# Optimization experiments

Measured on AMD Instinct MI355X. Metric: run time of the kernel, lower is better.

The kernel has to match this reference:

```python
import jax, jax.numpy as jnp
import numpy as np

B, N, E, ATT, TT, IT = 32, 5000, 500, 50, 4, 24
TEMP = 0.5

def leaky(x):
    return jnp.where(x > 0, x, 0.1 * x)

def ln(x, g, b, eps=1e-5):
    m = jnp.mean(x, axis=-1, keepdims=True)
    v = jnp.mean((x - m) ** 2, axis=-1, keepdims=True)
    return (x - m) * jax.lax.rsqrt(v + eps) * g + b

def setup_inputs() -> dict:
    key = jax.random.key(0)
    ks = jax.random.split(key, 16)
    s = 0.05
    return {
        'positive_sample': jax.random.randint(ks[0], (B, 3), 0, N),
        'ent_text_emb': jax.random.normal(ks[1], (N, TT, 384), jnp.float32),
        'ent_img_emb': jax.random.normal(ks[2], (N, IT, 383), jnp.float32),
        'entity_embedding': jax.random.normal(ks[3], (N, E), jnp.float32) * s,
        'relation_embedding': jax.random.normal(ks[4], (N, E), jnp.float32) * s,
        'W_text': jax.random.normal(ks[5], (ATT, 384), jnp.float32) * s,
        'b_text': jnp.zeros((ATT,), jnp.float32),
        'W_img': jax.random.normal(ks[6], (ATT, 383), jnp.float32) * s,
        'b_img': jnp.zeros((ATT,), jnp.float32),
        'W_tproj': jax.random.normal(ks[7], (ATT, ATT * IT), jnp.float32) * s,
        'b_tproj': jnp.zeros((ATT,), jnp.float32),
        'W_iproj': jax.random.normal(ks[8], (ATT, ATT * TT), jnp.float32) * s,
        'b_iproj': jnp.zeros((ATT,), jnp.float32),
        'W_rel1': jax.random.normal(ks[9], (IT * TT, E), jnp.float32) * s,
        'b_rel1': jnp.zeros((IT * TT,), jnp.float32),
        'W_rel2': jax.random.normal(ks[10], (IT * TT, E), jnp.float32) * s,
        'b_rel2': jnp.zeros((IT * TT,), jnp.float32),
        'W1': jax.random.normal(ks[11], (100, 2 * E), jnp.float32) * s,
        'b1': jnp.zeros((100,), jnp.float32),
        'W3': jax.random.normal(ks[12], (E, 100), jnp.float32) * s,
        'b3': jnp.zeros((E,), jnp.float32),
        'ln_g': jnp.ones((ATT,), jnp.float32),
        'ln_b': jnp.zeros((ATT,), jnp.float32),
    }

def _cos_sim(X, p):
    # X [B,N,d], p [B,d]; denominators are detached as in the torch code
    num = jnp.einsum('bnd,bd->bn', X, p)
    den = jnp.linalg.norm(X, axis=2) * jnp.linalg.norm(p, axis=1)[:, None]
    return num / (jax.lax.stop_gradient(den) + 1e-10)

def reference(positive_sample, ent_text_emb, ent_img_emb, entity_embedding,
              relation_embedding, W_text, b_text, W_img, b_img, W_tproj, b_tproj,
              W_iproj, b_iproj, W_rel1, b_rel1, W_rel2, b_rel2, W1, b1, W3, b3,
              ln_g, ln_b):
    rel = relation_embedding[positive_sample[:, 1]]              # [B,E]
    text_emb = leaky(jnp.einsum('ntf,df->ntd', ent_text_emb, W_text) + b_text)  # [N,4,50]
    img_emb = leaky(jnp.einsum('nif,df->nid', ent_img_emb, W_img) + b_img)      # [N,24,50]
    cross = jnp.einsum('nid,ntd->nit', img_emb, text_emb)        # [N,24,4]

    # image branch: softmax over img tokens, plus relation-gated path
    img_att = jnp.einsum('nti,nid->ntd', jax.nn.softmax(cross.transpose(0, 2, 1), axis=2), img_emb)  # [N,4,50]
    rg_i = jax.nn.sigmoid(rel @ W_rel1.T + b_rel1).reshape(B, IT, TT)           # [B,24,4]
    gated_i = rg_i[:, None] * cross[None]                                        # [B,N,24,4]
    img_att_rg = jnp.einsum('bnit,nid->bntd', gated_i, img_emb)                  # [B,N,4,50]
    img_att_all = ln(img_att_rg, ln_g, ln_b) + ln(img_att, ln_g, ln_b)[None]
    img_att_all = img_att_all.reshape(B, N, TT * ATT) @ W_iproj.T + b_iproj      # [B,N,50]

    # text branch: softmax over text tokens, plus relation-gated path
    text_att = jnp.einsum('nit,ntd->nid', jax.nn.softmax(cross, axis=2), text_emb)  # [N,24,50]
    rg_t = jax.nn.sigmoid(rel @ W_rel2.T + b_rel2).reshape(B, IT, TT)
    gated_t = rg_t[:, None] * cross[None]                                        # [B,N,24,4]
    text_att_rg = jnp.einsum('bnit,ntd->bnid', gated_t, text_emb)                # [B,N,24,50]
    text_att_all = ln(text_att_rg, ln_g, ln_b) + ln(text_att, ln_g, ln_b)[None]
    text_att_all = text_att_all.reshape(B, N, IT * ATT) @ W_tproj.T + b_tproj    # [B,N,50]

    # structural gate on KGE entity embeddings (split W1 to avoid concat)
    h = leaky(entity_embedding @ W1[:, :E].T[None].squeeze(0).T.T  # placeholder removed below
              ) if False else None
    h = leaky((entity_embedding @ W1[:, :E].T)[None] + (rel @ W1[:, E:].T)[:, None] + b1)  # [B,N,100]
    gate = jax.nn.sigmoid(h @ W3.T + b3)                                         # [B,N,E]
    t_att = entity_embedding[None] * gate                                        # [B,N,E]

    pos_idx = positive_sample[:, 2]  # tail-batch
    bi = jnp.arange(B)
    pos_img = img_att_all[bi, pos_idx]    # [B,50]
    pos_text = text_att_all[bi, pos_idx]  # [B,50]
    pos_t = t_att[bi, pos_idx]            # [B,E]

    simil_img = _cos_sim(img_att_all, pos_img)
    simil_text = _cos_sim(text_att_all, pos_text)
    simil_t = _cos_sim(t_att, pos_t)

    out = (jax.nn.softmax(simil_t / TEMP, axis=1)
           + jax.nn.softmax(simil_img / TEMP, axis=1)
           + jax.nn.softmax(simil_text / TEMP, axis=1))
    return (out, simil_img, simil_text, simil_t)
```

## Files before the change

### kernel.cpp

```cpp
#include <hip/hip_runtime.h>
#include <math.h>

#define BB 32
#define NN 5000
#define EE 500
#define AT 50
#define TTT 4
#define ITT 24
#define FT 384
#define FI 383
#define KH 100
#define BN (BB*NN)

__device__ __forceinline__ float leaky(float x){ return x > 0.f ? x : 0.1f*x; }
__device__ __forceinline__ float sigm(float x){ return 1.f/(1.f+__expf(-x)); }

enum : size_t {
  O_WTT = 0,
  O_WIT = 19968,
  O_WIP = 39936,
  O_WTP = 50336,
  O_W1T = 112736,
  O_W3T = 162736,
  O_SIP = 212736,
  O_STP = 212944,
  O_CBI = 214192,
  O_CBT = 214244,
  O_RGI = 214296,
  O_RGT = 217368,
  O_RB  = 220440,
  O_A   = 223640,
  O_PT  = 723640,
  O_PTN = 739640,
  O_PIM = 739672,
  O_PIMN= 741336,
  O_PTX = 741368,
  O_PTXN= 743032,
  O_MR  = 743064,
  O_SR  = 743160,
  O_EMB = 743256,
};

__global__ void k_prep(const float* Wt, const float* Wi, const float* Wip, const float* Wtp,
                       const float* W1, const float* W3, const float* g, const float* lb,
                       const float* bip, const float* btp, float* ws){
  int id = blockIdx.x*256 + threadIdx.x;
  if (id < 19968){ int f=id/52, d=id%52; ws[O_WTT+id] = (d<50)? Wt[d*FT+f] : 0.f; return; }
  id -= 19968;
  if (id < 19968){ int f=id/52, d=id%52; ws[O_WIT+id] = (f<383 && d<50)? Wi[d*FI+f] : 0.f; return; }
  id -= 19968;
  if (id < 10400){ int m=id/52, o=id%52; int t=m/50, d=m%50;
                   ws[O_WIP+id] = (o<50)? Wip[o*200+t*50+d]*g[d] : 0.f; return; }
  id -= 10400;
  if (id < 62400){ int m=id/52, o=id%52; int i=m/50, d=m%50;
                   ws[O_WTP+id] = (o<50)? Wtp[o*1200+i*50+d]*g[d] : 0.f; return; }
  id -= 62400;
  if (id < 50000){ int e=id/100, k=id%100; ws[O_W1T+id] = W1[k*1000+e]; return; }
  id -= 50000;
  if (id < 50000){ int k=id/500, e=id%500; ws[O_W3T+id] = W3[e*100+k]; return; }
  id -= 50000;
  if (id < 208){ int t=id/52, o=id%52; float s=0;
                 if (o<50) for(int d=0;d<50;d++) s += Wip[o*200+t*50+d]*g[d];
                 ws[O_SIP+id]=s; return; }
  id -= 208;
  if (id < 1248){ int i=id/52, o=id%52; float s=0;
                  if (o<50) for(int d=0;d<50;d++) s += Wtp[o*1200+i*50+d]*g[d];
                  ws[O_STP+id]=s; return; }
  id -= 1248;
  if (id < 52){ int o=id; float s=0;
                if (o<50){ for(int j=0;j<200;j++) s += lb[j%50]*Wip[o*200+j]; s=2.f*s+bip[o]; }
                ws[O_CBI+o]=s; return; }
  id -= 52;
  if (id < 52){ int o=id; float s=0;
                if (o<50){ for(int j=0;j<1200;j++) s += lb[j%50]*Wtp[o*1200+j]; s=2.f*s+btp[o]; }
                ws[O_CBT+o]=s; return; }
}

__global__ void k_rel(const int* ps, const float* rele, const float* Wr1, const float* br1,
                      const float* Wr2, const float* br2, const float* W1, float* ws){
  __shared__ float relL[EE];
  int b = blockIdx.x;
  int r = ps[b*3+1];
  for (int e=threadIdx.x; e<EE; e+=256) relL[e] = rele[(size_t)r*EE+e];
  __syncthreads();
  for (int j=threadIdx.x; j<292; j+=256){
    if (j<96){
      float a=br1[j]; const float* w=&Wr1[j*EE];
      for(int e=0;e<EE;e++) a+=relL[e]*w[e];
      ws[O_RGI+b*96+j]=sigm(a);
    } else if (j<192){
      int jj=j-96; float a=br2[jj]; const float* w=&Wr2[jj*EE];
      for(int e=0;e<EE;e++) a+=relL[e]*w[e];
      ws[O_RGT+b*96+jj]=sigm(a);
    } else {
      int k=j-192; float a=0; const float* w=&W1[k*1000+500];
      for(int e=0;e<EE;e++) a+=relL[e]*w[e];
      ws[O_RB+b*100+k]=a;
    }
  }
}

__global__ void k_A(const float* ent, float* ws){
  __shared__ float entL[8*EE];
  int n0 = blockIdx.x*8;
  for (int idx=threadIdx.x; idx<8*EE; idx+=256) entL[idx] = ent[(size_t)n0*EE + idx];
  __syncthreads();
  const float* W1T = &ws[O_W1T];
  for (int idx=threadIdx.x; idx<800; idx+=256){
    int rr=idx/100, k=idx%100; float a=0;
    const float* el=&entL[rr*EE];
    for (int e=0;e<EE;e++) a += el[e]*W1T[e*100+k];
    ws[O_A + (size_t)(n0+rr)*100 + k] = a;
  }
}

__global__ void k_pos(const int* ps, const float* ent, const float* b1, const float* b3, float* ws){
  __shared__ float hL[KH];
  __shared__ float red[4];
  int b=blockIdx.x; int n=ps[b*3+2]; int tid=threadIdx.x;
  if (tid<KH) hL[tid] = leaky(ws[O_A+(size_t)n*100+tid] + ws[O_RB+b*100+tid] + b1[tid]);
  __syncthreads();
  const float* w3t=&ws[O_W3T];
  float sq=0;
  for (int e=tid; e<EE; e+=256){
    float a=b3[e];
    for (int k=0;k<KH;k++) a += hL[k]*w3t[k*500+e];
    float gg=sigm(a); float ta=ent[(size_t)n*EE+e]*gg;
    ws[O_PT+b*500+e]=ta; sq+=ta*ta;
  }
  for (int off=1; off<64; off<<=1) sq += __shfl_xor(sq, off);
  if ((tid&63)==0) red[tid>>6]=sq;
  __syncthreads();
  if (tid==0) ws[O_PTN+b] = sqrtf(red[0]+red[1]+red[2]+red[3]);
}

__global__ __launch_bounds__(256) void k_emb(const float* X, const float* Wp, const float* bias,
                                             float* emb, int R, int F, int rowsPerN, int rowOff,
                                             int xstride){
  __shared__ __align__(16) float Wl[128*52];
  int row = blockIdx.x*256 + threadIdx.x;
  bool act = row < R;
  float4 acc[13];
  #pragma unroll
  for (int c=0;c<13;c++) acc[c]=make_float4(0,0,0,0);
  const float* xr = X + (size_t)(act?row:0)*xstride;
  for (int f0=0; f0<F; f0+=128){
    int nf = min(128, F-f0);
    __syncthreads();
    for (int j=threadIdx.x; j<nf*52; j+=256) Wl[j] = Wp[(size_t)f0*52 + j];
    __syncthreads();
    if (act){
      for (int f=0; f<nf; ++f){
        float x = xr[f0+f];
        const float4* wr = (const float4*)&Wl[f*52];
        #pragma unroll
        for (int c=0;c<13;++c){
          float4 w=wr[c];
          acc[c].x+=x*w.x; acc[c].y+=x*w.y; acc[c].z+=x*w.z; acc[c].w+=x*w.w;
        }
      }
    }
  }
  if (act){
    int n = row / rowsPerN, rr = row % rowsPerN;
    float* dst = emb + (size_t)n*1456 + (size_t)(rowOff+rr)*52;
    #pragma unroll
    for (int c=0;c<13;++c){
      float4 v=acc[c]; int o=c*4;
      v.x=leaky(v.x+bias[o]); v.y=leaky(v.y+bias[o+1]);
      if (c<12){ v.z=leaky(v.z+bias[o+2]); v.w=leaky(v.w+bias[o+3]); }
      else { v.z=0.f; v.w=0.f; }
      *(float4*)&dst[o]=v;
    }
  }
}

__global__ __launch_bounds__(256) void k_main(const int* ps, float* ws, float* out, int mode){
  __shared__ __align__(16) float teie[1456];
  __shared__ __align__(16) float Pm[120*52];
  __shared__ __align__(16) float Um[120*32];
  __shared__ __align__(16) float Gi[576];
  __shared__ __align__(16) float crs[96];
  __shared__ __align__(16) float aimg[96], atxt[96];
  __shared__ __align__(16) float part1[96], part2[96];
  __shared__ __align__(16) float aU[120];
  __shared__ __align__(16) float PattC[52], QattC[52];
  __shared__ float Gts[16], mimg[24], mtxt[4];
  __shared__ float muA1[4], muA2[24];
  __shared__ float accD1[32], accN1[32], accD2[32], accN2[32];

  int tid = threadIdx.x;
  int bstar = blockIdx.x;
  int n = mode ? ps[bstar*3+2] : blockIdx.x;

  const float* embn = &ws[O_EMB + (size_t)n*1456];
  for (int j=tid; j<364; j+=256) *(float4*)&teie[j*4] = *(const float4*)&embn[j*4];
  if (tid<32){ accD1[tid]=0.f; accN1[tid]=0.f; accD2[tid]=0.f; accN2[tid]=0.f; }
  __syncthreads();

  for (int it=tid; it<716; it+=256){
    if (it<576){
      int i=it/24, j=it%24; float s=0;
      const float* a=&teie[(4+i)*52]; const float* b=&teie[(4+j)*52];
      for(int d=0;d<50;d++) s+=a[d]*b[d];
      Gi[it]=s;
    } else if (it<672){
      int c=it-576; int i=c>>2, t=c&3; float s=0;
      const float* a=&teie[(4+i)*52]; const float* b=&teie[t*52];
      for(int d=0;d<50;d++) s+=a[d]*b[d];
      crs[c]=s;
    } else if (it<688){
      int c=it-672; int t=c>>2, u=c&3; float s=0;
      const float* a=&teie[t*52]; const float* b=&teie[u*52];
      for(int d=0;d<50;d++) s+=a[d]*b[d];
      Gts[c]=s;
    } else if (it<712){
      int i=it-688; float s=0; const float* a=&teie[(4+i)*52];
      for(int d=0;d<50;d++) s+=a[d];
      mimg[i]=s*0.02f;
    } else {
      int t=it-712; float s=0; const float* a=&teie[t*52];
      for(int d=0;d<50;d++) s+=a[d];
      mtxt[t]=s*0.02f;
    }
  }
  __syncthreads();

  if (tid<4){
    int t=tid;
    float mx=-1e30f; for(int i=0;i<24;i++) mx=fmaxf(mx,crs[i*4+t]);
    float ex[24]; float s=0;
    for(int i=0;i<24;i++){ ex[i]=__expf(crs[i*4+t]-mx); s+=ex[i]; }
    float inv=1.f/s; float mu=0;
    for(int i=0;i<24;i++){ float a=ex[i]*inv; aimg[i*4+t]=a; mu+=a*mimg[i]; }
    muA1[t]=mu;
  } else if (tid>=64 && tid<88){
    int i=tid-64;
    float mx=-1e30f; for(int t=0;t<4;t++) mx=fmaxf(mx,crs[i*4+t]);
    float ex[4]; float s=0;
    for(int t=0;t<4;t++){ ex[t]=__expf(crs[i*4+t]-mx); s+=ex[t]; }
    float inv=1.f/s; float mu=0;
    for(int t=0;t<4;t++){ float a=ex[t]*inv; atxt[i*4+t]=a; mu+=a*mtxt[t]; }
    muA2[i]=mu;
  }
  __syncthreads();

  const float* WIPg=&ws[O_WIP];
  for (int it=tid; it<1248; it+=256){
    int z=it/13, q=it%13; int t=z/24, i=z%24;
    const float* wb=&WIPg[(size_t)(t*50)*52 + q*4];
    const float* ieb=&teie[(4+i)*52];
    float4 a=make_float4(0,0,0,0);
    for (int d=0; d<50; ++d){
      float e=ieb[d];
      float4 w=*(const float4*)&wb[(size_t)d*52];
      a.x+=e*w.x; a.y+=e*w.y; a.z+=e*w.z; a.w+=e*w.w;
    }
    *(float4*)&Pm[z*52+q*4]=a;
  }
  for (int j=tid; j<208; j+=256) Pm[96*52+j]=ws[O_SIP+j];
  if (tid<96){
    int i=tid>>2, t=tid&3;
    float s=0; for(int j=0;j<24;j++) s+=Gi[i*24+j]*aimg[j*4+t];
    part1[tid]=aimg[tid]*s;
  } else if (tid<192){
    int c=tid-96; int t=c&3;
    float s=0; for(int u=0;u<4;u++) s+=Gts[t*4+u]*atxt[(c&~3)+u];
    part2[c]=atxt[c]*s;
  }
  __syncthreads();

  if (tid<128){
    int b=tid&31, t=tid>>5;
    float w1r[24];
    for(int i=0;i<24;i++) w1r[i]=ws[O_RGI+b*96+i*4+t]*crs[i*4+t];
    float mu=0; for(int i=0;i<24;i++) mu+=w1r[i]*mimg[i];
    float q=0;
    for(int i=0;i<24;i++){ float s=0; for(int j=0;j<24;j++) s+=Gi[i*24+j]*w1r[j]; q+=w1r[i]*s; }
    float inv=rsqrtf(q*0.02f-mu*mu+1e-5f);
    for(int i=0;i<24;i++) Um[(t*24+i)*32+b]=inv*w1r[i];
    Um[(96+t)*32+b]=-inv*mu;
  } else if (tid<228){
    int z=tid-128;
    int t=(z<96)? (z/24) : (z-96);
    float q=0; for(int i=0;i<24;i++) q+=part1[i*4+t];
    float inv=rsqrtf(q*0.02f-muA1[t]*muA1[t]+1e-5f);
    aU[z]=(z<96)? inv*aimg[(z%24)*4+t] : -inv*muA1[t];
  }
  __syncthreads();

  if (tid<52){
    float s=ws[O_CBI+tid];
    for(int z=0;z<100;z++) s+=aU[z]*Pm[z*52+tid];
    PattC[tid]=s;
  }
  __syncthreads();

  {
    int b=tid&31, q0=tid>>5;
    bool h2=(q0+8)<13;
    float4 a0=make_float4(0,0,0,0), a1=make_float4(0,0,0,0);
    #pragma unroll 4
    for (int z=0; z<100; ++z){
      float u=Um[z*32+b];
      float4 p0=*(const float4*)&Pm[z*52+q0*4];
      a0.x+=u*p0.x; a0.y+=u*p0.y; a0.z+=u*p0.z; a0.w+=u*p0.w;
      if (h2){
        float4 p1=*(const float4*)&Pm[z*52+(q0+8)*4];
        a1.x+=u*p1.x; a1.y+=u*p1.y; a1.z+=u*p1.z; a1.w+=u*p1.w;
      }
    }
    float4 c0=*(const float4*)&PattC[q0*4];
    a0.x+=c0.x; a0.y+=c0.y; a0.z+=c0.z; a0.w+=c0.w;
    if (h2){ float4 c1=*(const float4*)&PattC[(q0+8)*4]; a1.x+=c1.x; a1.y+=c1.y; a1.z+=c1.z; a1.w+=c1.w; }
    float ni=a0.x*a0.x+a0.y*a0.y+a0.z*a0.z+a0.w*a0.w;
    if (h2) ni+=a1.x*a1.x+a1.y*a1.y+a1.z*a1.z+a1.w*a1.w;
    if (!mode){
      const float* pv=&ws[O_PIM+b*52];
      float4 p0=*(const float4*)&pv[q0*4];
      float di=a0.x*p0.x+a0.y*p0.y+a0.z*p0.z+a0.w*p0.w;
      if (h2){
        float4 p1=*(const float4*)&pv[(q0+8)*4];
        di+=a1.x*p1.x+a1.y*p1.y+a1.z*p1.z+a1.w*p1.w;
      }
      atomicAdd(&accD1[b],di); atomicAdd(&accN1[b],ni);
    } else {
      atomicAdd(&accN1[b],ni);
      if (b==bstar){
        *(float4*)&ws[O_PIM+b*52+q0*4]=a0;
        if (h2) *(float4*)&ws[O_PIM+b*52+(q0+8)*4]=a1;
      }
    }
  }
  __syncthreads();

  if (!mode){
    if (tid<32)
      out[(size_t)BN + (size_t)tid*NN + n] = accD1[tid]/(sqrtf(accN1[tid])*ws[O_PIMN+tid]+1e-10f);
  } else {
    if (tid==0) ws[O_PIMN+bstar]=sqrtf(accN1[bstar]);
  }
  {
    const float* WTPg=&ws[O_WTP];
    for (int it=tid; it<1248; it+=256){
      int z=it/13, q=it%13; int t=z/24, i=z%24;
      const float* wb=&WTPg[(size_t)(i*50)*52 + q*4];
      const float* teb=&teie[t*52];
      float4 a=make_float4(0,0,0,0);
      for (int d=0; d<50; ++d){
        float e=teb[d];
        float4 w=*(const float4*)&wb[(size_t)d*52];
        a.x+=e*w.x; a.y+=e*w.y; a.z+=e*w.z; a.w+=e*w.w;
      }
      *(float4*)&Pm[z*52+q*4]=a;
    }
    for (int j=tid; j<1248; j+=256) Pm[96*52+j]=ws[O_STP+j];
  }
  __syncthreads();

  for (int it=tid; it<888; it+=256){
    if (it<768){
      int b=it&31, i=it>>5;
      float w2r[4];
      for(int t=0;t<4;t++) w2r[t]=ws[O_RGT+b*96+i*4+t]*crs[i*4+t];
      float mu=0; for(int t=0;t<4;t++) mu+=w2r[t]*mtxt[t];
      float q=0;
      for(int t=0;t<4;t++){ float s=0; for(int u=0;u<4;u++) s+=Gts[t*4+u]*w2r[u]; q+=w2r[t]*s; }
      float inv=rsqrtf(q*0.02f-mu*mu+1e-5f);
      for(int t=0;t<4;t++) Um[(t*24+i)*32+b]=inv*w2r[t];
      Um[(96+i)*32+b]=-inv*mu;
    } else {
      int z=it-768;
      int i=(z<96)? (z%24) : (z-96);
      float q=0; for(int t=0;t<4;t++) q+=part2[i*4+t];
      float inv=rsqrtf(q*0.02f-muA2[i]*muA2[i]+1e-5f);
      aU[z]=(z<96)? inv*atxt[(z%24)*4+(z/24)] : -inv*muA2[i];
    }
  }
  __syncthreads();

  if (tid<52){
    float s=ws[O_CBT+tid];
    for(int z=0;z<120;z++) s+=aU[z]*Pm[z*52+tid];
    QattC[tid]=s;
  }
  __syncthreads();

  {
    int b=tid&31, q0=tid>>5;
    bool h2=(q0+8)<13;
    float4 a0=make_float4(0,0,0,0), a1=make_float4(0,0,0,0);
    #pragma unroll 4
    for (int z=0; z<120; ++z){
      float u=Um[z*32+b];
      float4 p0=*(const float4*)&Pm[z*52+q0*4];
      a0.x+=u*p0.x; a0.y+=u*p0.y; a0.z+=u*p0.z; a0.w+=u*p0.w;
      if (h2){
        float4 p1=*(const float4*)&Pm[z*52+(q0+8)*4];
        a1.x+=u*p1.x; a1.y+=u*p1.y; a1.z+=u*p1.z; a1.w+=u*p1.w;
      }
    }
    float4 c0=*(const float4*)&QattC[q0*4];
    a0.x+=c0.x; a0.y+=c0.y; a0.z+=c0.z; a0.w+=c0.w;
    if (h2){ float4 c1=*(const float4*)&QattC[(q0+8)*4]; a1.x+=c1.x; a1.y+=c1.y; a1.z+=c1.z; a1.w+=c1.w; }
    float ni=a0.x*a0.x+a0.y*a0.y+a0.z*a0.z+a0.w*a0.w;
    if (h2) ni+=a1.x*a1.x+a1.y*a1.y+a1.z*a1.z+a1.w*a1.w;
    if (!mode){
      const float* pv=&ws[O_PTX+b*52];
      float4 p0=*(const float4*)&pv[q0*4];
      float di=a0.x*p0.x+a0.y*p0.y+a0.z*p0.z+a0.w*p0.w;
      if (h2){
        float4 p1=*(const float4*)&pv[(q0+8)*4];
        di+=a1.x*p1.x+a1.y*p1.y+a1.z*p1.z+a1.w*p1.w;
      }
      atomicAdd(&accD2[b],di); atomicAdd(&accN2[b],ni);
    } else {
      atomicAdd(&accN2[b],ni);
      if (b==bstar){
        *(float4*)&ws[O_PTX+b*52+q0*4]=a0;
        if (h2) *(float4*)&ws[O_PTX+b*52+(q0+8)*4]=a1;
      }
    }
  }
  __syncthreads();

  if (!mode){
    if (tid<32)
      out[2*(size_t)BN + (size_t)tid*NN + n] = accD2[tid]/(sqrtf(accN2[tid])*ws[O_PTXN+tid]+1e-10f);
  } else {
    if (tid==0) ws[O_PTXN+bstar]=sqrtf(accN2[bstar]);
  }
}

__global__ __launch_bounds__(256) void k_gate(const float* ent, const float* b1, const float* b3,
                                              float* ws, float* out){
  __shared__ float entL[EE];
  __shared__ float b3L[EE];
  __shared__ __align__(16) float hallT[KH*32];
  __shared__ __align__(16) float w3c[KH*100];
  __shared__ __align__(16) float PTc[BB*100];
  __shared__ float numL[BB], sqL[BB];
  int n=blockIdx.x, tid=threadIdx.x;

  for (int e=tid; e<EE; e+=256){ entL[e]=ent[(size_t)n*EE+e]; b3L[e]=b3[e]; }
  if (tid<BB){ numL[tid]=0.f; sqL[tid]=0.f; }
  for (int idx=tid; idx<KH*32; idx+=256){
    int k=idx>>5, b=idx&31;
    hallT[idx] = leaky(ws[O_A+(size_t)n*KH+k] + ws[O_RB+b*KH+k] + b1[k]);
  }

  int eslot=tid&31, bslot=tid>>5;
  bool val = eslot<25;
  int j0 = (val? eslot:0)*4;
  float pn0=0,pn1=0,pn2=0,pn3=0, ps0=0,ps1=0,ps2=0,ps3=0;
  const float* W3T=&ws[O_W3T];
  const float* PT=&ws[O_PT];

  for (int c=0;c<5;c++){
    __syncthreads();
    for (int idx=tid; idx<10000; idx+=256){
      int k=idx/100, j=idx%100;
      w3c[idx]=W3T[(size_t)k*500 + c*100 + j];
    }
    for (int idx=tid; idx<3200; idx+=256){
      int b=idx/100, j=idx%100;
      PTc[idx]=PT[(size_t)b*EE + c*100 + j];
    }
    __syncthreads();

    float4 a0=make_float4(0,0,0,0), a1=make_float4(0,0,0,0);
    float4 a2=make_float4(0,0,0,0), a3=make_float4(0,0,0,0);
    const float4* wr=(const float4*)&w3c[j0];
    const float4* hr=(const float4*)&hallT[bslot*4];
    #pragma unroll 4
    for (int k=0;k<KH;k++){
      float4 w=wr[(size_t)k*25];
      float4 h=hr[(size_t)k*8];
      a0.x+=h.x*w.x; a0.y+=h.x*w.y; a0.z+=h.x*w.z; a0.w+=h.x*w.w;
      a1.x+=h.y*w.x; a1.y+=h.y*w.y; a1.z+=h.y*w.z; a1.w+=h.y*w.w;
      a2.x+=h.z*w.x; a2.y+=h.z*w.y; a2.z+=h.z*w.z; a2.w+=h.z*w.w;
      a3.x+=h.w*w.x; a3.y+=h.w*w.y; a3.z+=h.w*w.z; a3.w+=h.w*w.w;
    }
    if (val){
      float4 bb4=*(const float4*)&b3L[c*100+j0];
      float4 ee4=*(const float4*)&entL[c*100+j0];
      float4 p0=*(const float4*)&PTc[(bslot*4+0)*100+j0];
      float4 p1=*(const float4*)&PTc[(bslot*4+1)*100+j0];
      float4 p2=*(const float4*)&PTc[(bslot*4+2)*100+j0];
      float4 p3=*(const float4*)&PTc[(bslot*4+3)*100+j0];
      float t;
      t=ee4.x*sigm(a0.x+bb4.x); pn0+=t*p0.x; ps0+=t*t;
      t=ee4.y*sigm(a0.y+bb4.y); pn0+=t*p0.y; ps0+=t*t;
      t=ee4.z*sigm(a0.z+bb4.z); pn0+=t*p0.z; ps0+=t*t;
      t=ee4.w*sigm(a0.w+bb4.w); pn0+=t*p0.w; ps0+=t*t;
      t=ee4.x*sigm(a1.x+bb4.x); pn1+=t*p1.x; ps1+=t*t;
      t=ee4.y*sigm(a1.y+bb4.y); pn1+=t*p1.y; ps1+=t*t;
      t=ee4.z*sigm(a1.z+bb4.z); pn1+=t*p1.z; ps1+=t*t;
      t=ee4.w*sigm(a1.w+bb4.w); pn1+=t*p1.w; ps1+=t*t;
      t=ee4.x*sigm(a2.x+bb4.x); pn2+=t*p2.x; ps2+=t*t;
      t=ee4.y*sigm(a2.y+bb4.y); pn2+=t*p2.y; ps2+=t*t;
      t=ee4.z*sigm(a2.z+bb4.z); pn2+=t*p2.z; ps2+=t*t;
      t=ee4.w*sigm(a2.w+bb4.w); pn2+=t*p2.w; ps2+=t*t;
      t=ee4.x*sigm(a3.x+bb4.x); pn3+=t*p3.x; ps3+=t*t;
      t=ee4.y*sigm(a3.y+bb4.y); pn3+=t*p3.y; ps3+=t*t;
      t=ee4.z*sigm(a3.z+bb4.z); pn3+=t*p3.z; ps3+=t*t;
      t=ee4.w*sigm(a3.w+bb4.w); pn3+=t*p3.w; ps3+=t*t;
    }
  }
  for (int off=1; off<32; off<<=1){
    pn0+=__shfl_xor(pn0,off); ps0+=__shfl_xor(ps0,off);
    pn1+=__shfl_xor(pn1,off); ps1+=__shfl_xor(ps1,off);
    pn2+=__shfl_xor(pn2,off); ps2+=__shfl_xor(ps2,off);
    pn3+=__shfl_xor(pn3,off); ps3+=__shfl_xor(ps3,off);
  }
  if (eslot==0){
    int b0=bslot*4;
    atomicAdd(&numL[b0+0],pn0); atomicAdd(&sqL[b0+0],ps0);
    atomicAdd(&numL[b0+1],pn1); atomicAdd(&sqL[b0+1],ps1);
    atomicAdd(&numL[b0+2],pn2); atomicAdd(&sqL[b0+2],ps2);
    atomicAdd(&numL[b0+3],pn3); atomicAdd(&sqL[b0+3],ps3);
  }
  __syncthreads();
  if (tid<BB){
    out[3*(size_t)BN + (size_t)tid*NN + n] = numL[tid]/(sqrtf(sqL[tid])*ws[O_PTN+tid]+1e-10f);
  }
}

__global__ void k_smax1(const float* out, float* ws){
  __shared__ float red[4];
  __shared__ float Msh;
  int a=blockIdx.x>>5, b=blockIdx.x&31, tid=threadIdx.x;
  const float* arr=&out[(size_t)(1+a)*BN + (size_t)b*NN];
  float mx=-1e30f;
  for (int i=tid;i<NN;i+=256) mx=fmaxf(mx,arr[i]);
  for (int off=1;off<64;off<<=1) mx=fmaxf(mx,__shfl_xor(mx,off));
  if ((tid&63)==0) red[tid>>6]=mx;
  __syncthreads();
  if (tid==0) Msh=fmaxf(fmaxf(red[0],red[1]),fmaxf(red[2],red[3]));
  __syncthreads();
  float M2=2.f*Msh;
  float s=0;
  for (int i=tid;i<NN;i+=256) s+=__expf(2.f*arr[i]-M2);
  for (int off=1;off<64;off<<=1) s+=__shfl_xor(s,off);
  if ((tid&63)==0) red[tid>>6]=s;
  __syncthreads();
  if (tid==0){ ws[O_MR+a*32+b]=M2; ws[O_SR+a*32+b]=red[0]+red[1]+red[2]+red[3]; }
}

__global__ void k_smax2(float* out, const float* ws){
  int t=blockIdx.x*256+threadIdx.x;
  if (t>=BN) return;
  int b=t/NN;
  float r=0;
  for (int a=0;a<3;a++)
    r += __expf(2.f*out[(size_t)(1+a)*BN+t]-ws[O_MR+a*32+b])/ws[O_SR+a*32+b];
  out[t]=r;
}

extern "C" void kernel_launch(void* const* d_in, const int* in_sizes, int n_in,
                              void* d_out, int out_size, void* d_ws, size_t ws_size,
                              hipStream_t stream){
  (void)in_sizes; (void)n_in; (void)out_size; (void)ws_size;
  const int*   ps  =(const int*)  d_in[0];
  const float* etg =(const float*)d_in[1];
  const float* eig =(const float*)d_in[2];
  const float* ent =(const float*)d_in[3];
  const float* rele=(const float*)d_in[4];
  const float* Wt  =(const float*)d_in[5];
  const float* btx =(const float*)d_in[6];
  const float* Wi  =(const float*)d_in[7];
  const float* bim =(const float*)d_in[8];
  const float* Wtp =(const float*)d_in[9];
  const float* btp =(const float*)d_in[10];
  const float* Wip =(const float*)d_in[11];
  const float* bip =(const float*)d_in[12];
  const float* Wr1 =(const float*)d_in[13];
  const float* br1 =(const float*)d_in[14];
  const float* Wr2 =(const float*)d_in[15];
  const float* br2 =(const float*)d_in[16];
  const float* W1  =(const float*)d_in[17];
  const float* b1  =(const float*)d_in[18];
  const float* W3  =(const float*)d_in[19];
  const float* b3  =(const float*)d_in[20];
  const float* lng =(const float*)d_in[21];
  const float* lnb =(const float*)d_in[22];
  float* ws =(float*)d_ws;
  float* out=(float*)d_out;

  k_prep <<<838,256,0,stream>>>(Wt,Wi,Wip,Wtp,W1,W3,lng,lnb,bip,btp,ws);
  k_rel  <<<32, 256,0,stream>>>(ps,rele,Wr1,br1,Wr2,br2,W1,ws);
  k_A    <<<625,256,0,stream>>>(ent,ws);
  k_pos  <<<32, 256,0,stream>>>(ps,ent,b1,b3,ws);
  k_emb  <<<79, 256,0,stream>>>(etg,&ws[O_WTT],btx,&ws[O_EMB],20000,FT,4,0,FT);
  k_emb  <<<469,256,0,stream>>>(eig,&ws[O_WIT],bim,&ws[O_EMB],120000,FI,24,4,FI);
  k_main <<<32,  256,0,stream>>>(ps,ws,out,1);
  k_main <<<5000,256,0,stream>>>(ps,ws,out,0);
  k_gate <<<5000,256,0,stream>>>(ent,b1,b3,ws,out);
  k_smax1<<<96, 256,0,stream>>>(out,ws);
  k_smax2<<<625,256,0,stream>>>(out,ws);
}
```

Measured before the change: 1.776 ms.

## Retile gate kernel over batch and 64-entity tiles with transposed A layout

```diff
diff --git a/kernel.cpp b/kernel.cpp
--- a/kernel.cpp
+++ b/kernel.cpp
@@ -110,7 +110,7 @@
     int rr=idx/100, k=idx%100; float a=0;
     const float* el=&entL[rr*EE];
     for (int e=0;e<EE;e++) a += el[e]*W1T[e*100+k];
-    ws[O_A + (size_t)(n0+rr)*100 + k] = a;
+    ws[O_A + (size_t)k*NN + (n0+rr)] = a;
   }
 }
 
@@ -118,7 +118,7 @@
   __shared__ float hL[KH];
   __shared__ float red[4];
   int b=blockIdx.x; int n=ps[b*3+2]; int tid=threadIdx.x;
-  if (tid<KH) hL[tid] = leaky(ws[O_A+(size_t)n*100+tid] + ws[O_RB+b*100+tid] + b1[tid]);
+  if (tid<KH) hL[tid] = leaky(ws[O_A+(size_t)tid*NN+n] + ws[O_RB+b*100+tid] + b1[tid]);
   __syncthreads();
   const float* w3t=&ws[O_W3T];
   float sq=0;
@@ -434,95 +434,103 @@
 
 __global__ __launch_bounds__(256) void k_gate(const float* ent, const float* b1, const float* b3,
                                               float* ws, float* out){
-  __shared__ float entL[EE];
-  __shared__ float b3L[EE];
-  __shared__ __align__(16) float hallT[KH*32];
-  __shared__ __align__(16) float w3c[KH*100];
-  __shared__ __align__(16) float PTc[BB*100];
-  __shared__ float numL[BB], sqL[BB];
-  int n=blockIdx.x, tid=threadIdx.x;
-
-  for (int e=tid; e<EE; e+=256){ entL[e]=ent[(size_t)n*EE+e]; b3L[e]=b3[e]; }
-  if (tid<BB){ numL[tid]=0.f; sqL[tid]=0.f; }
-  for (int idx=tid; idx<KH*32; idx+=256){
-    int k=idx>>5, b=idx&31;
-    hallT[idx] = leaky(ws[O_A+(size_t)n*KH+k] + ws[O_RB+b*KH+k] + b1[k]);
-  }
-
-  int eslot=tid&31, bslot=tid>>5;
-  bool val = eslot<25;
-  int j0 = (val? eslot:0)*4;
-  float pn0=0,pn1=0,pn2=0,pn3=0, ps0=0,ps1=0,ps2=0,ps3=0;
-  const float* W3T=&ws[O_W3T];
-  const float* PT=&ws[O_PT];
-
-  for (int c=0;c<5;c++){
-    __syncthreads();
-    for (int idx=tid; idx<10000; idx+=256){
-      int k=idx/100, j=idx%100;
-      w3c[idx]=W3T[(size_t)k*500 + c*100 + j];
-    }
-    for (int idx=tid; idx<3200; idx+=256){
-      int b=idx/100, j=idx%100;
-      PTc[idx]=PT[(size_t)b*EE + c*100 + j];
-    }
-    __syncthreads();
-
-    float4 a0=make_float4(0,0,0,0), a1=make_float4(0,0,0,0);
-    float4 a2=make_float4(0,0,0,0), a3=make_float4(0,0,0,0);
-    const float4* wr=(const float4*)&w3c[j0];
-    const float4* hr=(const float4*)&hallT[bslot*4];
-    #pragma unroll 4
-    for (int k=0;k<KH;k++){
-      float4 w=wr[(size_t)k*25];
-      float4 h=hr[(size_t)k*8];
-      a0.x+=h.x*w.x; a0.y+=h.x*w.y; a0.z+=h.x*w.z; a0.w+=h.x*w.w;
-      a1.x+=h.y*w.x; a1.y+=h.y*w.y; a1.z+=h.y*w.z; a1.w+=h.y*w.w;
-      a2.x+=h.z*w.x; a2.y+=h.z*w.y; a2.z+=h.z*w.z; a2.w+=h.z*w.w;
-      a3.x+=h.w*w.x; a3.y+=h.w*w.y; a3.z+=h.w*w.z; a3.w+=h.w*w.w;
-    }
-    if (val){
-      float4 bb4=*(const float4*)&b3L[c*100+j0];
-      float4 ee4=*(const float4*)&entL[c*100+j0];
-      float4 p0=*(const float4*)&PTc[(bslot*4+0)*100+j0];
-      float4 p1=*(const float4*)&PTc[(bslot*4+1)*100+j0];
-      float4 p2=*(const float4*)&PTc[(bslot*4+2)*100+j0];
-      float4 p3=*(const float4*)&PTc[(bslot*4+3)*100+j0];
-      float t;
-      t=ee4.x*sigm(a0.x+bb4.x); pn0+=t*p0.x; ps0+=t*t;
-      t=ee4.y*sigm(a0.y+bb4.y); pn0+=t*p0.y; ps0+=t*t;
-      t=ee4.z*sigm(a0.z+bb4.z); pn0+=t*p0.z; ps0+=t*t;
-      t=ee4.w*sigm(a0.w+bb4.w); pn0+=t*p0.w; ps0+=t*t;
-      t=ee4.x*sigm(a1.x+bb4.x); pn1+=t*p1.x; ps1+=t*t;
-      t=ee4.y*sigm(a1.y+bb4.y); pn1+=t*p1.y; ps1+=t*t;
-      t=ee4.z*sigm(a1.z+bb4.z); pn1+=t*p1.z; ps1+=t*t;
-      t=ee4.w*sigm(a1.w+bb4.w); pn1+=t*p1.w; ps1+=t*t;
-      t=ee4.x*sigm(a2.x+bb4.x); pn2+=t*p2.x; ps2+=t*t;
-      t=ee4.y*sigm(a2.y+bb4.y); pn2+=t*p2.y; ps2+=t*t;
-      t=ee4.z*sigm(a2.z+bb4.z); pn2+=t*p2.z; ps2+=t*t;
-      t=ee4.w*sigm(a2.w+bb4.w); pn2+=t*p2.w; ps2+=t*t;
-      t=ee4.x*sigm(a3.x+bb4.x); pn3+=t*p3.x; ps3+=t*t;
-      t=ee4.y*sigm(a3.y+bb4.y); pn3+=t*p3.y; ps3+=t*t;
-      t=ee4.z*sigm(a3.z+bb4.z); pn3+=t*p3.z; ps3+=t*t;
-      t=ee4.w*sigm(a3.w+bb4.w); pn3+=t*p3.w; ps3+=t*t;
-    }
-  }
+  __shared__ __align__(16) float hL[50*68];
+  __shared__ __align__(16) float wc[50*128];
+  __shared__ __align__(16) float PTb[512];
+  __shared__ __align__(16) float b3L[512];
+  __shared__ float rbL[KH];
+
+  int tid = threadIdx.x;
+  int b   = blockIdx.x & 31;
+  int n0  = (blockIdx.x >> 5) * 64;
+
+  for (int j=tid; j<512; j+=256){
+    PTb[j] = (j<EE)? ws[O_PT + b*EE + j] : 0.f;
+    b3L[j] = (j<EE)? b3[j] : 0.f;
+  }
+  if (tid < KH) rbL[tid] = ws[O_RB + b*KH + tid] + b1[tid];
+
+  int ej = tid & 31;
+  int ni = tid >> 5;
+
+  float pn[8], ps[8];
+  #pragma unroll
+  for (int r=0;r<8;r++){ pn[r]=0.f; ps[r]=0.f; }
+
+  for (int ec=0; ec<4; ++ec){
+    int e0 = ec*128;
+    float4 acc[8];
+    #pragma unroll
+    for (int r=0;r<8;r++) acc[r]=make_float4(0,0,0,0);
+
+    for (int kh=0; kh<2; ++kh){
+      __syncthreads();
+      for (int idx=tid; idx<1600; idx+=256){
+        int k = idx>>5, j4 = idx&31;
+        int e = e0 + j4*4;
+        float4 v = make_float4(0,0,0,0);
+        if (e+3 < EE) v = *(const float4*)&ws[O_W3T + (size_t)(kh*50+k)*EE + e];
+        *(float4*)&wc[k*128 + j4*4] = v;
+      }
+      for (int idx=tid; idx<3200; idx+=256){
+        int k = idx>>6, nn = idx&63;
+        int n = n0 + nn;
+        float v = 0.f;
+        if (n < NN) v = leaky(ws[O_A + (size_t)(kh*50+k)*NN + n] + rbL[kh*50+k]);
+        hL[k*68 + nn] = v;
+      }
+      __syncthreads();
+
+      const float4* wp = (const float4*)&wc[ej*4];
+      const float4* hp = (const float4*)&hL[ni*8];
+      #pragma unroll 2
+      for (int k=0;k<50;k++){
+        float4 w  = wp[k*32];
+        float4 h0 = hp[k*17];
+        float4 h1 = hp[k*17 + 1];
+        acc[0].x+=h0.x*w.x; acc[0].y+=h0.x*w.y; acc[0].z+=h0.x*w.z; acc[0].w+=h0.x*w.w;
+        acc[1].x+=h0.y*w.x; acc[1].y+=h0.y*w.y; acc[1].z+=h0.y*w.z; acc[1].w+=h0.y*w.w;
+        acc[2].x+=h0.z*w.x; acc[2].y+=h0.z*w.y; acc[2].z+=h0.z*w.z; acc[2].w+=h0.z*w.w;
+        acc[3].x+=h0.w*w.x; acc[3].y+=h0.w*w.y; acc[3].z+=h0.w*w.z; acc[3].w+=h0.w*w.w;
+        acc[4].x+=h1.x*w.x; acc[4].y+=h1.x*w.y; acc[4].z+=h1.x*w.z; acc[4].w+=h1.x*w.w;
+        acc[5].x+=h1.y*w.x; acc[5].y+=h1.y*w.y; acc[5].z+=h1.y*w.z; acc[5].w+=h1.y*w.w;
+        acc[6].x+=h1.z*w.x; acc[6].y+=h1.z*w.y; acc[6].z+=h1.z*w.z; acc[6].w+=h1.z*w.w;
+        acc[7].x+=h1.w*w.x; acc[7].y+=h1.w*w.y; acc[7].z+=h1.w*w.z; acc[7].w+=h1.w*w.w;
+      }
+    }
+
+    {
+      int ebase = e0 + ej*4;
+      bool ev = (ebase + 3) < EE;
+      float4 bb = *(const float4*)&b3L[ebase];
+      float4 pt = *(const float4*)&PTb[ebase];
+      #pragma unroll
+      for (int r=0;r<8;r++){
+        int n = n0 + ni*8 + r;
+        float4 en = make_float4(0,0,0,0);
+        if (ev && n < NN) en = *(const float4*)&ent[(size_t)n*EE + ebase];
+        float t0 = en.x * sigm(acc[r].x + bb.x);
+        float t1 = en.y * sigm(acc[r].y + bb.y);
+        float t2 = en.z * sigm(acc[r].z + bb.z);
+        float t3 = en.w * sigm(acc[r].w + bb.w);
+        pn[r] += t0*pt.x + t1*pt.y + t2*pt.z + t3*pt.w;
+        ps[r] += t0*t0 + t1*t1 + t2*t2 + t3*t3;
+      }
+    }
+  }
+
   for (int off=1; off<32; off<<=1){
-    pn0+=__shfl_xor(pn0,off); ps0+=__shfl_xor(ps0,off);
-    pn1+=__shfl_xor(pn1,off); ps1+=__shfl_xor(ps1,off);
-    pn2+=__shfl_xor(pn2,off); ps2+=__shfl_xor(ps2,off);
-    pn3+=__shfl_xor(pn3,off); ps3+=__shfl_xor(ps3,off);
-  }
-  if (eslot==0){
-    int b0=bslot*4;
-    atomicAdd(&numL[b0+0],pn0); atomicAdd(&sqL[b0+0],ps0);
-    atomicAdd(&numL[b0+1],pn1); atomicAdd(&sqL[b0+1],ps1);
-    atomicAdd(&numL[b0+2],pn2); atomicAdd(&sqL[b0+2],ps2);
-    atomicAdd(&numL[b0+3],pn3); atomicAdd(&sqL[b0+3],ps3);
-  }
-  __syncthreads();
-  if (tid<BB){
-    out[3*(size_t)BN + (size_t)tid*NN + n] = numL[tid]/(sqrtf(sqL[tid])*ws[O_PTN+tid]+1e-10f);
+    #pragma unroll
+    for (int r=0;r<8;r++){ pn[r]+=__shfl_xor(pn[r],off); ps[r]+=__shfl_xor(ps[r],off); }
+  }
+  if (ej==0){
+    float ptn = ws[O_PTN+b];
+    #pragma unroll
+    for (int r=0;r<8;r++){
+      int n = n0 + ni*8 + r;
+      if (n < NN)
+        out[3*(size_t)BN + (size_t)b*NN + n] = pn[r]/(sqrtf(ps[r])*ptn + 1e-10f);
+    }
   }
 }
 
@@ -595,7 +603,7 @@
   k_emb  <<<469,256,0,stream>>>(eig,&ws[O_WIT],bim,&ws[O_EMB],120000,FI,24,4,FI);
   k_main <<<32,  256,0,stream>>>(ps,ws,out,1);
   k_main <<<5000,256,0,stream>>>(ps,ws,out,0);
-  k_gate <<<5000,256,0,stream>>>(ent,b1,b3,ws,out);
+  k_gate <<<32*79,256,0,stream>>>(ent,b1,b3,ws,out);
   k_smax1<<<96, 256,0,stream>>>(out,ws);
   k_smax2<<<625,256,0,stream>>>(out,ws);
 }
```

New measurement: 1.549 ms. 1.15x faster.
